# Performance work log

Hardware: AMD Instinct MI355X
Metric: run time of the kernel (lower is better)

## Reference

```python
import jax, jax.numpy as jnp
import numpy as np

B, C, H, W = 32, 3, 512, 512
EPS = 1e-8


def _radius_bins(h, w):
    cy, cx = h // 2, w // 2
    y = jnp.arange(h, dtype=jnp.float32) - cy
    x = jnp.arange(w, dtype=jnp.float32) - cx
    radius = jnp.sqrt(y[:, None] ** 2 + x[None, :] ** 2)  # [H, W]
    max_r = min(cy, cx)
    bins = jnp.floor(radius).astype(jnp.int32)
    # pixels with radius >= max_r fall outside all bins in the original loop;
    # route them to a dummy overflow bin that we drop afterwards.
    bins = jnp.where(bins < max_r, bins, max_r)
    return bins.reshape(-1), max_r


def _psd(x):
    f = jnp.fft.fft2(x)                  # over last two dims, like torch.fft.fft2
    psd = jnp.abs(f) ** 2
    return jnp.log(psd + EPS)            # log_power=True


def _radial_average(psd):
    b, c, h, w = psd.shape
    bins, max_r = _radius_bins(h, w)     # [H*W], static
    data = psd.reshape(b * c, h * w).T   # [H*W, B*C]
    sums = jax.ops.segment_sum(data, bins, num_segments=max_r + 1)
    counts = jax.ops.segment_sum(jnp.ones((h * w,), psd.dtype), bins,
                                 num_segments=max_r + 1)
    avg = jnp.where(counts[:, None] > 0, sums / counts[:, None], 0.0)
    avg = avg[:max_r]                    # drop overflow bin -> [max_r, B*C]
    return avg.T.reshape(b, c, max_r)


def setup_inputs() -> dict:
    key = jax.random.key(0)
    k1, k2 = jax.random.split(key)
    predicted = jax.random.normal(k1, (B, C, H, W), dtype=jnp.float32)
    target = jax.random.normal(k2, (B, C, H, W), dtype=jnp.float32)
    return {"predicted": predicted, "target": target}


def reference(predicted, target):
    pred_rad = _radial_average(_psd(predicted))
    targ_rad = _radial_average(_psd(target))
    return jnp.mean(jnp.abs(pred_rad - targ_rad))  # l1, reduction='mean'
```

## Files before the change

kernel.cpp:

```cpp
#include <hip/hip_runtime.h>
#include <math.h>

#define HH 512
#define WW 512
#define IMG (HH*WW)
#define NIMG_PER 96
#define NIMG 192
#define NBIN 256
#define EPSV 1e-8f

#define CSTR 264
#define IMGC (512*CSTR)
#define NTILE 33
#define SLOT 580

__device__ __forceinline__ int drev(int s) {
    return ((s & 7) << 6) | (s & 56) | (s >> 6);
}
__device__ __forceinline__ int fsw(int a) { return a + (a >> 3); }

__device__ __forceinline__ float2 cmul(float2 a, float2 b) {
    return make_float2(a.x*b.x - a.y*b.y, a.x*b.y + a.y*b.x);
}
#define C_ADD(a,b) make_float2((a).x+(b).x, (a).y+(b).y)
#define C_SUB(a,b) make_float2((a).x-(b).x, (a).y-(b).y)
#define C_NI(a)    make_float2((a).y, -(a).x)

__device__ __forceinline__ void bfly8(float2 x[8]) {
    const float R = 0.70710678118654752440f;
    float2 t0=C_ADD(x[0],x[4]), t4=C_SUB(x[0],x[4]);
    float2 t1=C_ADD(x[1],x[5]), t5=C_SUB(x[1],x[5]);
    float2 t2=C_ADD(x[2],x[6]), t6=C_SUB(x[2],x[6]);
    float2 t3=C_ADD(x[3],x[7]), t7=C_SUB(x[3],x[7]);
    float2 u0=C_ADD(t0,t2), u2=C_SUB(t0,t2);
    float2 u1=C_ADD(t1,t3), u3=C_SUB(t1,t3);
    x[0]=C_ADD(u0,u1); x[4]=C_SUB(u0,u1);
    {
        float2 n3 = C_NI(u3);
        x[2]=C_ADD(u2,n3); x[6]=C_SUB(u2,n3);
    }
    float2 s1 = make_float2(R*(t5.x + t5.y), R*(t5.y - t5.x));
    float2 s2 = C_NI(t6);
    float2 s3 = make_float2(R*(t7.y - t7.x), -R*(t7.x + t7.y));
    float2 v0=C_ADD(t4,s2), v2=C_SUB(t4,s2);
    float2 v1=C_ADD(s1,s3), v3=C_SUB(s1,s3);
    x[1]=C_ADD(v0,v1); x[5]=C_SUB(v0,v1);
    {
        float2 n3 = C_NI(v3);
        x[3]=C_ADD(v2,n3); x[7]=C_SUB(v2,n3);
    }
}

__device__ __forceinline__ void twiddle7(float2* x, float base, float den) {
    float sn, cs;
    sincosf(-6.28318530717958647692f * base / den, &sn, &cs);
    float2 w1 = make_float2(cs, sn), w = w1;
    x[1] = cmul(x[1], w);
    #pragma unroll
    for (int j = 2; j < 8; ++j) { w = cmul(w, w1); x[j] = cmul(x[j], w); }
}

__global__ __launch_bounds__(256) void rowfft_kernel(
    const float* __restrict__ pred, const float* __restrict__ targ,
    float2* __restrict__ out, int img_base)
{
    __shared__ float LB[4640];
    float* sre = LB;
    float* sim = LB + 4*SLOT;
    const int t = threadIdx.x;

    const int pb = blockIdx.x;
    const int li = blockIdx.y;
    const int g  = img_base + li;
    const float* img = (g < NIMG_PER) ? (pred + (size_t)g * IMG)
                                      : (targ + (size_t)(g - NIMG_PER) * IMG);
    const float4* src4 = (const float4*)(img + (size_t)(pb*8) * WW);

    #pragma unroll
    for (int it = 0; it < 4; ++it) {
        const int id = it*256 + t;
        const int r  = id >> 7;
        const int x4 = id & 127;
        const float4 v = src4[id];
        float* dst = ((r & 1) ? sim : sre) + (r >> 1) * SLOT;
        const int b = 4*x4 + (x4 >> 1);
        dst[b+0]=v.x; dst[b+1]=v.y; dst[b+2]=v.z; dst[b+3]=v.w;
    }
    __syncthreads();

    const int i    = t & 63;
    const int slot = t >> 6;
    float* re = sre + slot*SLOT;
    float* im = sim + slot*SLOT;
    float2 x[8];

    #pragma unroll
    for (int j = 0; j < 8; ++j) { int a = fsw(i + 64*j); x[j] = make_float2(re[a], im[a]); }
    bfly8(x);
    twiddle7(x, (float)i, 512.0f);
    #pragma unroll
    for (int j = 0; j < 8; ++j) { int a = fsw(i + 64*j); re[a] = x[j].x; im[a] = x[j].y; }
    __syncthreads();

    const int grp = i >> 3, i2 = i & 7;
    #pragma unroll
    for (int j = 0; j < 8; ++j) { int a = fsw(64*grp + i2 + 8*j); x[j] = make_float2(re[a], im[a]); }
    bfly8(x);
    twiddle7(x, (float)i2, 64.0f);
    #pragma unroll
    for (int j = 0; j < 8; ++j) { int a = fsw(64*grp + i2 + 8*j); re[a] = x[j].x; im[a] = x[j].y; }
    __syncthreads();

    #pragma unroll
    for (int j = 0; j < 8; ++j) { int a = fsw(8*i + j); x[j] = make_float2(re[a], im[a]); }
    bfly8(x);
    #pragma unroll
    for (int j = 0; j < 8; ++j) { int a = fsw(8*i + j); re[a] = x[j].x; im[a] = x[j].y; }
    __syncthreads();

    const int w_ = t >> 6;
    int k;
    if (w_ > 0) k = ((t & 7) << 6) | (t & 56) | w_;
    else        k = (t < 32) ? (8*t + 4) : (8*(t - 32));
    const int kk = (k <= 256) ? k : (512 - k);
    const int a1 = fsw(drev(kk));
    const int a2 = (t == 0) ? fsw(drev(256)) : fsw(drev(512 - kk));

    float2 Fa[4], Fb[4], Qs[4];
    #pragma unroll
    for (int s = 0; s < 4; ++s) {
        const float Pr = sre[s*SLOT + a1], Pi2 = sim[s*SLOT + a1];
        const float Qr = sre[s*SLOT + a2], Qi  = sim[s*SLOT + a2];
        Fa[s] = make_float2(0.5f*(Pr+Qr), 0.5f*(Pi2-Qi));
        Fb[s] = make_float2(0.5f*(Pi2+Qi), 0.5f*(Qr-Pr));
        if (t == 0) {
            Fa[s] = make_float2(Pr, 0.0f);
            Fb[s] = make_float2(Pi2, 0.0f);
        }
        Qs[s] = make_float2(Qr, Qi);
    }
    __syncthreads();

    {
        const int fb = fsw(kk);
        #pragma unroll
        for (int s = 0; s < 4; ++s) {
            LB[(4*s+0)*290 + fb] = Fa[s].x;
            LB[(4*s+1)*290 + fb] = Fa[s].y;
            LB[(4*s+2)*290 + fb] = Fb[s].x;
            LB[(4*s+3)*290 + fb] = Fb[s].y;
        }
    }
    if (t == 0) {
        const int fb = fsw(256);
        #pragma unroll
        for (int s = 0; s < 4; ++s) {
            LB[(4*s+0)*290 + fb] = Qs[s].x;
            LB[(4*s+1)*290 + fb] = 0.0f;
            LB[(4*s+2)*290 + fb] = Qs[s].y;
            LB[(4*s+3)*290 + fb] = 0.0f;
        }
    }
    __syncthreads();

    float2* dst = out + (size_t)li * IMGC + (size_t)(pb*8) * CSTR;
    #pragma unroll
    for (int r = 0; r < 8; ++r) {
        const int pbase = (r >> 1)*4 + (r & 1)*2;
        float2* drow = dst + (size_t)r * CSTR;
        {
            const int fc = fsw(t);
            drow[t] = make_float2(LB[pbase*290 + fc], LB[(pbase+1)*290 + fc]);
        }
        if (t < 8) {
            const int c = 256 + t;
            float2 v = make_float2(0.0f, 0.0f);
            if (c == 256) {
                const int fc = fsw(256);
                v = make_float2(LB[pbase*290 + fc], LB[(pbase+1)*290 + fc]);
            }
            drow[c] = v;
        }
    }
}

__global__ __launch_bounds__(256) void colfft_kernel(
    const float2* __restrict__ in, float* __restrict__ bins, int img_base)
{
    __shared__ float sre[8*SLOT], sim[8*SLOT];
    __shared__ float bsum[NBIN];
    const int t = threadIdx.x;
    bsum[t] = 0.0f;

    const int li = blockIdx.y;
    const int x0 = blockIdx.x * 8;
    const float2* src = in + (size_t)li * IMGC;

    #pragma unroll
    for (int it = 0; it < 16; ++it) {
        const int id = it*256 + t;
        const int y  = id >> 3;
        const int cl = id & 7;
        const float2 v = src[(size_t)y * CSTR + (x0 + cl)];
        const int a = cl*SLOT + fsw(y);
        sre[a] = v.x; sim[a] = v.y;
    }
    __syncthreads();

    const int i  = t & 63;
    const int c0 = t >> 6;
    float2 x[2][8];

    #pragma unroll
    for (int sl = 0; sl < 2; ++sl) {
        float* re = sre + (c0 + 4*sl)*SLOT;
        float* im = sim + (c0 + 4*sl)*SLOT;
        #pragma unroll
        for (int j = 0; j < 8; ++j) { int a = fsw(i + 64*j); x[sl][j] = make_float2(re[a], im[a]); }
        bfly8(x[sl]);
    }
    {
        float sn, cs; sincosf(-6.28318530717958647692f * (float)i / 512.0f, &sn, &cs);
        float2 w1 = make_float2(cs, sn), w = w1;
        x[0][1] = cmul(x[0][1], w); x[1][1] = cmul(x[1][1], w);
        #pragma unroll
        for (int j = 2; j < 8; ++j) {
            w = cmul(w, w1);
            x[0][j] = cmul(x[0][j], w); x[1][j] = cmul(x[1][j], w);
        }
    }
    #pragma unroll
    for (int sl = 0; sl < 2; ++sl) {
        float* re = sre + (c0 + 4*sl)*SLOT;
        float* im = sim + (c0 + 4*sl)*SLOT;
        #pragma unroll
        for (int j = 0; j < 8; ++j) { int a = fsw(i + 64*j); re[a] = x[sl][j].x; im[a] = x[sl][j].y; }
    }
    __syncthreads();

    const int grp = i >> 3, i2 = i & 7;
    #pragma unroll
    for (int sl = 0; sl < 2; ++sl) {
        float* re = sre + (c0 + 4*sl)*SLOT;
        float* im = sim + (c0 + 4*sl)*SLOT;
        #pragma unroll
        for (int j = 0; j < 8; ++j) { int a = fsw(64*grp + i2 + 8*j); x[sl][j] = make_float2(re[a], im[a]); }
        bfly8(x[sl]);
    }
    {
        float sn, cs; sincosf(-6.28318530717958647692f * (float)i2 / 64.0f, &sn, &cs);
        float2 w1 = make_float2(cs, sn), w = w1;
        x[0][1] = cmul(x[0][1], w); x[1][1] = cmul(x[1][1], w);
        #pragma unroll
        for (int j = 2; j < 8; ++j) {
            w = cmul(w, w1);
            x[0][j] = cmul(x[0][j], w); x[1][j] = cmul(x[1][j], w);
        }
    }
    #pragma unroll
    for (int sl = 0; sl < 2; ++sl) {
        float* re = sre + (c0 + 4*sl)*SLOT;
        float* im = sim + (c0 + 4*sl)*SLOT;
        #pragma unroll
        for (int j = 0; j < 8; ++j) { int a = fsw(64*grp + i2 + 8*j); re[a] = x[sl][j].x; im[a] = x[sl][j].y; }
    }
    __syncthreads();

    #pragma unroll
    for (int sl = 0; sl < 2; ++sl) {
        const int cl = c0 + 4*sl;
        const int kx = x0 + cl;
        float* re = sre + cl*SLOT;
        float* im = sim + cl*SLOT;
        float2 y8[8];
        #pragma unroll
        for (int j = 0; j < 8; ++j) { int a = fsw(8*i + j); y8[j] = make_float2(re[a], im[a]); }
        bfly8(y8);
        if (kx <= 256) {
            const float wgt = (kx == 0 || kx == 256) ? 1.0f : 2.0f;
            const int dx = kx - 256;
            #pragma unroll
            for (int j = 0; j < 8; ++j) {
                const int q  = 8*i + j;
                const int ky = drev(q);
                const float val = __logf(y8[j].x*y8[j].x + y8[j].y*y8[j].y + EPSV);
                const int dy = ky - 256;
                const int b  = (int)sqrtf((float)(dy*dy + dx*dx));
                if (b < NBIN) atomicAdd(&bsum[b], wgt * val);
            }
        }
    }
    __syncthreads();

    atomicAdd(&bins[(size_t)(img_base + li) * NBIN + t], bsum[t]);
}

__global__ __launch_bounds__(256) void counts_kernel(float* __restrict__ cnt)
{
    __shared__ float c[NBIN];
    const int t = threadIdx.x;
    c[t] = 0.0f;
    __syncthreads();

    const int base = blockIdx.x * 4096;
    #pragma unroll
    for (int i = 0; i < 16; ++i) {
        const int id = base + i * 256 + t;
        const int y = id >> 9, xx = id & 511;
        const int dy = y - 256, dx = xx - 256;
        const int b  = (int)sqrtf((float)(dy*dy + dx*dx));
        if (b < NBIN) atomicAdd(&c[b], 1.0f);
    }
    __syncthreads();
    if (c[t] != 0.0f) atomicAdd(&cnt[t], c[t]);
}

__global__ __launch_bounds__(256) void finalize_kernel(
    const float* __restrict__ bins, const float* __restrict__ cnt,
    float* __restrict__ out)
{
    __shared__ float red[256];
    const int t = threadIdx.x;

    float acc = 0.0f;
    for (int id = t; id < NIMG_PER * NBIN; id += 256) {
        const int i = id >> 8;
        const int r = id & 255;
        const float d = fabsf(bins[(size_t)i * NBIN + r]
                            - bins[(size_t)(NIMG_PER + i) * NBIN + r]);
        acc += d / cnt[r];
    }
    red[t] = acc;
    __syncthreads();
    for (int w = 128; w > 0; w >>= 1) {
        if (t < w) red[t] += red[t + w];
        __syncthreads();
    }
    if (t == 0) out[0] = red[0] / (float)(NIMG_PER * NBIN);
}

extern "C" void kernel_launch(void* const* d_in, const int* in_sizes, int n_in,
                              void* d_out, int out_size, void* d_ws, size_t ws_size,
                              hipStream_t stream)
{
    const float* pred = (const float*)d_in[0];
    const float* targ = (const float*)d_in[1];
    float* out = (float*)d_out;

    char* ws = (char*)d_ws;
    float* bins = (float*)ws;
    float* cnt  = bins + (size_t)NIMG * NBIN;
    const size_t zero_bytes = ((size_t)NIMG * NBIN + NBIN) * sizeof(float);
    const size_t off = (zero_bytes + 255) & ~(size_t)255;
    float2* cbuf = (float2*)(ws + off);

    const size_t per_img = (size_t)IMGC * sizeof(float2);
    size_t avail = (ws_size > off) ? (ws_size - off) : 0;
    int chunk = (int)(avail / per_img);
    if (chunk > NIMG) chunk = NIMG;
    if (chunk < 1) chunk = 1;

    hipMemsetAsync(bins, 0, zero_bytes, stream);
    counts_kernel<<<dim3(64), dim3(256), 0, stream>>>(cnt);

    for (int base = 0; base < NIMG; base += chunk) {
        const int n = (NIMG - base < chunk) ? (NIMG - base) : chunk;
        dim3 gA(HH / 8, n), gB(NTILE, n), blk(256);
        rowfft_kernel<<<gA, blk, 0, stream>>>(pred, targ, cbuf, base);
        colfft_kernel<<<gB, blk, 0, stream>>>(cbuf, bins, base);
    }

    finalize_kernel<<<dim3(1), dim3(256), 0, stream>>>(bins, cnt, out);
}
```

Measured before the change: 256.8 us.

## Store row-FFT output transposed so column FFT reads contiguous columns

The row FFT kernel now writes its half-spectrum straight to global memory in a transposed [kx][y] layout using float4 stores. This removes the shared-memory staging pass and the extra barriers it needed. The column FFT kernel then reads each column contiguously, handles 4 columns per block instead of 8 across 65 tiles, and keeps one register set per thread. Twiddles now use fast __sinf/__cosf with directly computed powers instead of a chained product. The costs are lower trig accuracy, a scattered float4 write pattern in the row kernel, and more column blocks that each do less work.

```diff
diff --git a/kernel.cpp b/kernel.cpp
--- a/kernel.cpp
+++ b/kernel.cpp
@@ -9,10 +9,8 @@
 #define NBIN 256
 #define EPSV 1e-8f
 
-#define CSTR 264
-#define IMGC (512*CSTR)
-#define NTILE 33
-#define SLOT 580
+#define IMGC (257*512)
+#define SLOT 576
 
 __device__ __forceinline__ int drev(int s) {
     return ((s & 7) << 6) | (s & 56) | (s >> 6);
@@ -35,38 +33,35 @@
     float2 u0=C_ADD(t0,t2), u2=C_SUB(t0,t2);
     float2 u1=C_ADD(t1,t3), u3=C_SUB(t1,t3);
     x[0]=C_ADD(u0,u1); x[4]=C_SUB(u0,u1);
-    {
-        float2 n3 = C_NI(u3);
-        x[2]=C_ADD(u2,n3); x[6]=C_SUB(u2,n3);
-    }
+    { float2 n3 = C_NI(u3); x[2]=C_ADD(u2,n3); x[6]=C_SUB(u2,n3); }
     float2 s1 = make_float2(R*(t5.x + t5.y), R*(t5.y - t5.x));
     float2 s2 = C_NI(t6);
     float2 s3 = make_float2(R*(t7.y - t7.x), -R*(t7.x + t7.y));
     float2 v0=C_ADD(t4,s2), v2=C_SUB(t4,s2);
     float2 v1=C_ADD(s1,s3), v3=C_SUB(s1,s3);
     x[1]=C_ADD(v0,v1); x[5]=C_SUB(v0,v1);
-    {
-        float2 n3 = C_NI(v3);
-        x[3]=C_ADD(v2,n3); x[7]=C_SUB(v2,n3);
-    }
-}
-
-__device__ __forceinline__ void twiddle7(float2* x, float base, float den) {
-    float sn, cs;
-    sincosf(-6.28318530717958647692f * base / den, &sn, &cs);
-    float2 w1 = make_float2(cs, sn), w = w1;
-    x[1] = cmul(x[1], w);
-    #pragma unroll
-    for (int j = 2; j < 8; ++j) { w = cmul(w, w1); x[j] = cmul(x[j], w); }
+    { float2 n3 = C_NI(v3); x[3]=C_ADD(v2,n3); x[7]=C_SUB(v2,n3); }
+}
+
+__device__ __forceinline__ void twiddle7(float2* x, float ang) {
+    const float sn = __sinf(ang), cs = __cosf(ang);
+    const float2 w1 = make_float2(cs, sn);
+    const float2 w2 = cmul(w1, w1);
+    const float2 w3 = cmul(w2, w1);
+    const float2 w4 = cmul(w2, w2);
+    const float2 w5 = cmul(w2, w3);
+    const float2 w6 = cmul(w3, w3);
+    const float2 w7 = cmul(w3, w4);
+    x[1]=cmul(x[1],w1); x[2]=cmul(x[2],w2); x[3]=cmul(x[3],w3);
+    x[4]=cmul(x[4],w4); x[5]=cmul(x[5],w5); x[6]=cmul(x[6],w6);
+    x[7]=cmul(x[7],w7);
 }
 
 __global__ __launch_bounds__(256) void rowfft_kernel(
     const float* __restrict__ pred, const float* __restrict__ targ,
     float2* __restrict__ out, int img_base)
 {
-    __shared__ float LB[4640];
-    float* sre = LB;
-    float* sim = LB + 4*SLOT;
+    __shared__ float sre[4*SLOT], sim[4*SLOT];
     const int t = threadIdx.x;
 
     const int pb = blockIdx.x;
@@ -97,7 +92,7 @@
     #pragma unroll
     for (int j = 0; j < 8; ++j) { int a = fsw(i + 64*j); x[j] = make_float2(re[a], im[a]); }
     bfly8(x);
-    twiddle7(x, (float)i, 512.0f);
+    twiddle7(x, -0.012271846303085130f * (float)i);
     #pragma unroll
     for (int j = 0; j < 8; ++j) { int a = fsw(i + 64*j); re[a] = x[j].x; im[a] = x[j].y; }
     __syncthreads();
@@ -106,7 +101,7 @@
     #pragma unroll
     for (int j = 0; j < 8; ++j) { int a = fsw(64*grp + i2 + 8*j); x[j] = make_float2(re[a], im[a]); }
     bfly8(x);
-    twiddle7(x, (float)i2, 64.0f);
+    twiddle7(x, -0.098174770424681038f * (float)i2);
     #pragma unroll
     for (int j = 0; j < 8; ++j) { int a = fsw(64*grp + i2 + 8*j); re[a] = x[j].x; im[a] = x[j].y; }
     __syncthreads();
@@ -119,89 +114,48 @@
     __syncthreads();
 
     const int w_ = t >> 6;
-    int k;
-    if (w_ > 0) k = ((t & 7) << 6) | (t & 56) | w_;
-    else        k = (t < 32) ? (8*t + 4) : (8*(t - 32));
+    const int k  = (w_ > 0) ? (((t & 7) << 6) | (t & 56) | w_)
+                            : ((t < 32) ? (8*t + 4) : (8*(t - 32)));
     const int kk = (k <= 256) ? k : (512 - k);
     const int a1 = fsw(drev(kk));
-    const int a2 = (t == 0) ? fsw(drev(256)) : fsw(drev(512 - kk));
-
-    float2 Fa[4], Fb[4], Qs[4];
+    const int a2 = fsw(drev((512 - kk) & 511));
+
+    float4* dst = (float4*)out + (size_t)li * (IMGC/2) + (size_t)kk * 256 + pb*4;
     #pragma unroll
     for (int s = 0; s < 4; ++s) {
-        const float Pr = sre[s*SLOT + a1], Pi2 = sim[s*SLOT + a1];
-        const float Qr = sre[s*SLOT + a2], Qi  = sim[s*SLOT + a2];
-        Fa[s] = make_float2(0.5f*(Pr+Qr), 0.5f*(Pi2-Qi));
-        Fb[s] = make_float2(0.5f*(Pi2+Qi), 0.5f*(Qr-Pr));
-        if (t == 0) {
-            Fa[s] = make_float2(Pr, 0.0f);
-            Fb[s] = make_float2(Pi2, 0.0f);
-        }
-        Qs[s] = make_float2(Qr, Qi);
-    }
-    __syncthreads();
-
-    {
-        const int fb = fsw(kk);
+        const float Pr = sre[s*SLOT + a1], Pi = sim[s*SLOT + a1];
+        const float Qr = sre[s*SLOT + a2], Qi = sim[s*SLOT + a2];
+        dst[s] = make_float4(0.5f*(Pr+Qr), 0.5f*(Pi-Qi),
+                             0.5f*(Pi+Qi), 0.5f*(Qr-Pr));
+    }
+    if (t == 0) {
+        const int a3 = fsw(drev(256));
+        float4* d2 = (float4*)out + (size_t)li * (IMGC/2) + (size_t)256 * 256 + pb*4;
         #pragma unroll
-        for (int s = 0; s < 4; ++s) {
-            LB[(4*s+0)*290 + fb] = Fa[s].x;
-            LB[(4*s+1)*290 + fb] = Fa[s].y;
-            LB[(4*s+2)*290 + fb] = Fb[s].x;
-            LB[(4*s+3)*290 + fb] = Fb[s].y;
-        }
-    }
-    if (t == 0) {
-        const int fb = fsw(256);
-        #pragma unroll
-        for (int s = 0; s < 4; ++s) {
-            LB[(4*s+0)*290 + fb] = Qs[s].x;
-            LB[(4*s+1)*290 + fb] = 0.0f;
-            LB[(4*s+2)*290 + fb] = Qs[s].y;
-            LB[(4*s+3)*290 + fb] = 0.0f;
-        }
-    }
-    __syncthreads();
-
-    float2* dst = out + (size_t)li * IMGC + (size_t)(pb*8) * CSTR;
-    #pragma unroll
-    for (int r = 0; r < 8; ++r) {
-        const int pbase = (r >> 1)*4 + (r & 1)*2;
-        float2* drow = dst + (size_t)r * CSTR;
-        {
-            const int fc = fsw(t);
-            drow[t] = make_float2(LB[pbase*290 + fc], LB[(pbase+1)*290 + fc]);
-        }
-        if (t < 8) {
-            const int c = 256 + t;
-            float2 v = make_float2(0.0f, 0.0f);
-            if (c == 256) {
-                const int fc = fsw(256);
-                v = make_float2(LB[pbase*290 + fc], LB[(pbase+1)*290 + fc]);
-            }
-            drow[c] = v;
-        }
+        for (int s = 0; s < 4; ++s)
+            d2[s] = make_float4(sre[s*SLOT + a3], 0.0f, sim[s*SLOT + a3], 0.0f);
     }
 }
 
 __global__ __launch_bounds__(256) void colfft_kernel(
     const float2* __restrict__ in, float* __restrict__ bins, int img_base)
 {
-    __shared__ float sre[8*SLOT], sim[8*SLOT];
+    __shared__ float sre[4*SLOT], sim[4*SLOT];
     __shared__ float bsum[NBIN];
     const int t = threadIdx.x;
     bsum[t] = 0.0f;
 
     const int li = blockIdx.y;
-    const int x0 = blockIdx.x * 8;
+    const int x0 = blockIdx.x * 4;
     const float2* src = in + (size_t)li * IMGC;
 
     #pragma unroll
-    for (int it = 0; it < 16; ++it) {
-        const int id = it*256 + t;
-        const int y  = id >> 3;
-        const int cl = id & 7;
-        const float2 v = src[(size_t)y * CSTR + (x0 + cl)];
+    for (int it = 0; it < 8; ++it) {
+        const int cl = it >> 1;
+        const int kx = x0 + cl;
+        const int y  = ((it & 1) << 8) + t;
+        float2 v = make_float2(0.0f, 0.0f);
+        if (kx <= 256) v = src[(size_t)kx * 512 + y];
         const int a = cl*SLOT + fsw(y);
         sre[a] = v.x; sim[a] = v.y;
     }
@@ -209,73 +163,32 @@
 
     const int i  = t & 63;
     const int c0 = t >> 6;
-    float2 x[2][8];
-
-    #pragma unroll
-    for (int sl = 0; sl < 2; ++sl) {
-        float* re = sre + (c0 + 4*sl)*SLOT;
-        float* im = sim + (c0 + 4*sl)*SLOT;
+    float* re = sre + c0*SLOT;
+    float* im = sim + c0*SLOT;
+    float2 x[8];
+
+    #pragma unroll
+    for (int j = 0; j < 8; ++j) { int a = fsw(i + 64*j); x[j] = make_float2(re[a], im[a]); }
+    bfly8(x);
+    twiddle7(x, -0.012271846303085130f * (float)i);
+    #pragma unroll
+    for (int j = 0; j < 8; ++j) { int a = fsw(i + 64*j); re[a] = x[j].x; im[a] = x[j].y; }
+    __syncthreads();
+
+    const int grp = i >> 3, i2 = i & 7;
+    #pragma unroll
+    for (int j = 0; j < 8; ++j) { int a = fsw(64*grp + i2 + 8*j); x[j] = make_float2(re[a], im[a]); }
+    bfly8(x);
+    twiddle7(x, -0.098174770424681038f * (float)i2);
+    #pragma unroll
+    for (int j = 0; j < 8; ++j) { int a = fsw(64*grp + i2 + 8*j); re[a] = x[j].x; im[a] = x[j].y; }
+    __syncthreads();
+
+    {
+        const int kx = x0 + c0;
         #pragma unroll
-        for (int j = 0; j < 8; ++j) { int a = fsw(i + 64*j); x[sl][j] = make_float2(re[a], im[a]); }
-        bfly8(x[sl]);
-    }
-    {
-        float sn, cs; sincosf(-6.28318530717958647692f * (float)i / 512.0f, &sn, &cs);
-        float2 w1 = make_float2(cs, sn), w = w1;
-        x[0][1] = cmul(x[0][1], w); x[1][1] = cmul(x[1][1], w);
-        #pragma unroll
-        for (int j = 2; j < 8; ++j) {
-            w = cmul(w, w1);
-            x[0][j] = cmul(x[0][j], w); x[1][j] = cmul(x[1][j], w);
-        }
-    }
-    #pragma unroll
-    for (int sl = 0; sl < 2; ++sl) {
-        float* re = sre + (c0 + 4*sl)*SLOT;
-        float* im = sim + (c0 + 4*sl)*SLOT;
-        #pragma unroll
-        for (int j = 0; j < 8; ++j) { int a = fsw(i + 64*j); re[a] = x[sl][j].x; im[a] = x[sl][j].y; }
-    }
-    __syncthreads();
-
-    const int grp = i >> 3, i2 = i & 7;
-    #pragma unroll
-    for (int sl = 0; sl < 2; ++sl) {
-        float* re = sre + (c0 + 4*sl)*SLOT;
-        float* im = sim + (c0 + 4*sl)*SLOT;
-        #pragma unroll
-        for (int j = 0; j < 8; ++j) { int a = fsw(64*grp + i2 + 8*j); x[sl][j] = make_float2(re[a], im[a]); }
-        bfly8(x[sl]);
-    }
-    {
-        float sn, cs; sincosf(-6.28318530717958647692f * (float)i2 / 64.0f, &sn, &cs);
-        float2 w1 = make_float2(cs, sn), w = w1;
-        x[0][1] = cmul(x[0][1], w); x[1][1] = cmul(x[1][1], w);
-        #pragma unroll
-        for (int j = 2; j < 8; ++j) {
-            w = cmul(w, w1);
-            x[0][j] = cmul(x[0][j], w); x[1][j] = cmul(x[1][j], w);
-        }
-    }
-    #pragma unroll
-    for (int sl = 0; sl < 2; ++sl) {
-        float* re = sre + (c0 + 4*sl)*SLOT;
-        float* im = sim + (c0 + 4*sl)*SLOT;
-        #pragma unroll
-        for (int j = 0; j < 8; ++j) { int a = fsw(64*grp + i2 + 8*j); re[a] = x[sl][j].x; im[a] = x[sl][j].y; }
-    }
-    __syncthreads();
-
-    #pragma unroll
-    for (int sl = 0; sl < 2; ++sl) {
-        const int cl = c0 + 4*sl;
-        const int kx = x0 + cl;
-        float* re = sre + cl*SLOT;
-        float* im = sim + cl*SLOT;
-        float2 y8[8];
-        #pragma unroll
-        for (int j = 0; j < 8; ++j) { int a = fsw(8*i + j); y8[j] = make_float2(re[a], im[a]); }
-        bfly8(y8);
+        for (int j = 0; j < 8; ++j) { int a = fsw(8*i + j); x[j] = make_float2(re[a], im[a]); }
+        bfly8(x);
         if (kx <= 256) {
             const float wgt = (kx == 0 || kx == 256) ? 1.0f : 2.0f;
             const int dx = kx - 256;
@@ -283,7 +196,7 @@
             for (int j = 0; j < 8; ++j) {
                 const int q  = 8*i + j;
                 const int ky = drev(q);
-                const float val = __logf(y8[j].x*y8[j].x + y8[j].y*y8[j].y + EPSV);
+                const float val = __logf(x[j].x*x[j].x + x[j].y*x[j].y + EPSV);
                 const int dy = ky - 256;
                 const int b  = (int)sqrtf((float)(dy*dy + dx*dx));
                 if (b < NBIN) atomicAdd(&bsum[b], wgt * val);
@@ -365,7 +278,7 @@
 
     for (int base = 0; base < NIMG; base += chunk) {
         const int n = (NIMG - base < chunk) ? (NIMG - base) : chunk;
-        dim3 gA(HH / 8, n), gB(NTILE, n), blk(256);
+        dim3 gA(HH / 8, n), gB(65, n), blk(256);
         rowfft_kernel<<<gA, blk, 0, stream>>>(pred, targ, cbuf, base);
         colfft_kernel<<<gB, blk, 0, stream>>>(cbuf, bins, base);
     }
```

Result: slower. 291.6 us (+13.5%).
